# Optimization experiments

Hardware: AMD Instinct MI355X
Metric: run time of the kernel (lower is better)

The kernel has to match this reference:

```python
import jax, jax.numpy as jnp
import numpy as np
from jax import lax

C = 512
BN_EPS = 1e-5
GLN_EPS = 1e-8


def setup_inputs() -> dict:
    key = jax.random.key(0)
    ks = jax.random.split(key, 10)
    B, T = 16, 4000
    x = jax.random.normal(ks[0], (B, C, T), dtype=jnp.float32)
    # BatchNorm1d params (eval mode: affine + running stats)
    bn_gamma = jax.random.normal(ks[1], (C,), dtype=jnp.float32) * 0.1 + 1.0
    bn_beta = jax.random.normal(ks[2], (C,), dtype=jnp.float32) * 0.1
    bn_mean = jax.random.normal(ks[3], (C,), dtype=jnp.float32) * 0.1
    bn_var = jax.random.uniform(ks[4], (C,), dtype=jnp.float32) + 0.5
    # depthwise Conv1d(512,512,3,groups=512,bias=False): kernel [O=C, I=1, K=3]
    dw_w = jax.random.normal(ks[5], (C, 1, 3), dtype=jnp.float32) * (1.0 / np.sqrt(3.0))
    # PReLU default: single shared parameter init 0.25
    prelu_a = jnp.full((1,), 0.25, dtype=jnp.float32)
    # GlobalLayerNorm(512) affine params
    gln_gamma = jnp.ones((C,), dtype=jnp.float32)
    gln_beta = jnp.zeros((C,), dtype=jnp.float32)
    # pointwise Conv1d(512,512,1,bias=False): weight [O, I]
    pw_w = jax.random.normal(ks[6], (C, C), dtype=jnp.float32) * (1.0 / np.sqrt(C))
    return {"x": x, "bn_gamma": bn_gamma, "bn_beta": bn_beta, "bn_mean": bn_mean,
            "bn_var": bn_var, "dw_w": dw_w, "prelu_a": prelu_a,
            "gln_gamma": gln_gamma, "gln_beta": gln_beta, "pw_w": pw_w}


def reference(x, bn_gamma, bn_beta, bn_mean, bn_var, dw_w, prelu_a,
              gln_gamma, gln_beta, pw_w):
    # ReLU
    h = jax.nn.relu(x)
    # BatchNorm1d (eval mode, running stats), per-channel affine over [B,C,T]
    scale = (bn_gamma * lax.rsqrt(bn_var + BN_EPS))[None, :, None]
    h = h * scale + (bn_beta - bn_mean * bn_gamma * lax.rsqrt(bn_var + BN_EPS))[None, :, None]
    # depthwise conv1d, kernel 3, pad 1, groups=C
    h = lax.conv_general_dilated(h, dw_w, window_strides=(1,), padding=((1, 1),),
                                 feature_group_count=C,
                                 dimension_numbers=("NCH", "OIH", "NCH"))
    # PReLU (single shared slope)
    h = jnp.where(h >= 0, h, prelu_a[0] * h)
    # GlobalLayerNorm: normalize over (C, T) per sample, per-channel affine
    mean = jnp.mean(h, axis=(1, 2), keepdims=True)
    var = jnp.mean(jnp.square(h - mean), axis=(1, 2), keepdims=True)
    h = gln_gamma[None, :, None] * (h - mean) * lax.rsqrt(var + GLN_EPS) + gln_beta[None, :, None]
    # pointwise 1x1 conv == channel GEMM
    h = jnp.einsum("oc,bct->bot", pw_w, h)
    # residual
    return h + x
```

## Files before the change

kernel.cpp:

```cpp
#include <hip/hip_runtime.h>
#include <stdint.h>

#define B_ 16
#define C_ 512
#define T_ 4000
#define TPAD 4096

typedef float f32x4 __attribute__((ext_vector_type(4)));
typedef __bf16 bf16x8 __attribute__((ext_vector_type(8)));

__device__ inline unsigned short f2b(float f) {
  uint32_t u = __builtin_bit_cast(uint32_t, f);
  u = (u + 0x7fffu + ((u >> 16) & 1u)) >> 16;
  return (unsigned short)u;
}
__device__ inline float b2f(unsigned short h) {
  uint32_t u = ((uint32_t)h) << 16;
  return __builtin_bit_cast(float, u);
}
__device__ inline void gl_lds16(const void* g, void* s) {
  __builtin_amdgcn_global_load_lds(
      (const __attribute__((address_space(1))) uint32_t*)g,
      (__attribute__((address_space(3))) uint32_t*)s, 16, 0, 0);
}


__global__ void k_init(float* wsf) {
  int i = threadIdx.x;
  if (i < 32) wsf[i] = 0.f;
}

__global__ __launch_bounds__(64) void k_prepw(const float* __restrict__ pw,
                                              const float* __restrict__ gamma,
                                              const float* __restrict__ beta,
                                              unsigned short* __restrict__ Wp,
                                              float* __restrict__ wsf) {
  int o = blockIdx.x, l = threadIdx.x;
  float a1 = 0.f, a2 = 0.f;
  for (int j = 0; j < 8; ++j) {
    int c = j * 64 + l;
    float wv = pw[o * 512 + c];
    unsigned short wb = f2b(wv * gamma[c]);
    Wp[o * 512 + c] = wb;
    a1 += b2f(wb);
    a2 += wv * beta[c];
  }
  for (int s = 32; s > 0; s >>= 1) { a1 += __shfl_down(a1, s); a2 += __shfl_down(a2, s); }
  if (l == 0) { wsf[64 + o] = a1; wsf[576 + o] = a2; }
}

__global__ __launch_bounds__(512) void k_front(const float* __restrict__ x,
    const float* __restrict__ bng, const float* __restrict__ bnb,
    const float* __restrict__ bnm, const float* __restrict__ bnv,
    const float* __restrict__ dw, const float* __restrict__ pa,
    unsigned short* __restrict__ hT, float* __restrict__ wsf) {
  __shared__ unsigned short hs[256 * 128] __attribute__((aligned(16)));
  __shared__ float psc[128], pbi[128], pq0[128], pq1[128], pq2[128];
  __shared__ float partial[16];
  int tid = threadIdx.x;
  int l = tid & 63, w = tid >> 6;
  int tb = blockIdx.x;
  int cb = blockIdx.y;
  int b  = blockIdx.z;
  int t0 = tb * 256;
  if (tid < 128) {
    int c = cb * 128 + tid;
    float sc = bng[c] * rsqrtf(bnv[c] + 1e-5f);
    psc[tid] = sc;
    pbi[tid] = bnb[c] - bnm[c] * sc;
    pq0[tid] = dw[3 * c];
    pq1[tid] = dw[3 * c + 1];
    pq2[tid] = dw[3 * c + 2];
  }
  float alpha = pa[0];
  __syncthreads();

  int t = t0 + 4 * l;
  bool full = (t + 3 < T_);
  bool has_l = (t0 > 0);
  bool has_r = (t0 + 256 < T_);
  float sum = 0.f, sq = 0.f;
  int cs_x = (l & 7) << 3;

#pragma unroll 2
  for (int i = 0; i < 16; ++i) {
    int cl = w * 16 + i;
    const float* xr = x + ((size_t)b * C_ + cb * 128 + cl) * T_;
    float sc = psc[cl], bi = pbi[cl];
    float w0 = pq0[cl], w1 = pq1[cl], w2 = pq2[cl];
    f32x4 u;
    if (full) {
      const f32x4 v = *(const f32x4*)(xr + t);
      u.x = fmaxf(v.x, 0.f) * sc + bi;
      u.y = fmaxf(v.y, 0.f) * sc + bi;
      u.z = fmaxf(v.z, 0.f) * sc + bi;
      u.w = fmaxf(v.w, 0.f) * sc + bi;
    } else {
      u = (f32x4){0.f, 0.f, 0.f, 0.f};
    }
    float el = has_l ? (fmaxf(xr[t0 - 1], 0.f) * sc + bi) : 0.f;
    float er = has_r ? (fmaxf(xr[t0 + 256], 0.f) * sc + bi) : 0.f;
    float up = __shfl_up(u.w, 1);   if (l == 0)  up = el;
    float un = __shfl_down(u.x, 1); if (l == 63) un = er;
    float h[4];
    h[0] = w0 * up  + w1 * u.x + w2 * u.y;
    h[1] = w0 * u.x + w1 * u.y + w2 * u.z;
    h[2] = w0 * u.y + w1 * u.z + w2 * u.w;
    h[3] = w0 * u.z + w1 * u.w + w2 * un;
    int cs = cl ^ cs_x;
#pragma unroll
    for (int j = 0; j < 4; ++j) {
      float p = h[j] >= 0.f ? h[j] : alpha * h[j];
      if (!full) p = 0.f;
      sum += p; sq += p * p;
      hs[(4 * l + j) * 128 + cs] = f2b(p);
    }
  }

  for (int s = 32; s > 0; s >>= 1) { sum += __shfl_down(sum, s); sq += __shfl_down(sq, s); }
  if (l == 0) { partial[w] = sum; partial[8 + w] = sq; }
  __syncthreads();
  if (tid == 0) {
    float a = 0.f, c2 = 0.f;
    for (int k = 0; k < 8; ++k) { a += partial[k]; c2 += partial[8 + k]; }
    atomicAdd(&wsf[b], a);
    atomicAdd(&wsf[16 + b], c2);
  }

  unsigned short* dstb = hT + ((size_t)b * TPAD + t0) * 512 + cb * 128;
#pragma unroll
  for (int p = 0; p < 8; ++p) {
    int idx = p * 512 + tid;
    int tl = idx >> 4, g = idx & 15;
    int gs = g ^ ((tl >> 2) & 7);
    uint4 val = *(const uint4*)(hs + tl * 128 + gs * 8);
    *(uint4*)(dstb + (size_t)tl * 512 + g * 8) = val;
  }
}

__global__ void k_finalize(float* wsf) {
  int b = threadIdx.x;
  if (b < 16) {
    float n = (float)C_ * (float)T_;
    float mean = wsf[b] / n;
    float var = wsf[16 + b] / n - mean * mean;
    wsf[32 + b] = mean;
    wsf[48 + b] = rsqrtf(fmaxf(var, 0.f) + 1e-8f);
  }
}

__global__ __launch_bounds__(512, 2) void k_gemm(const unsigned short* __restrict__ Wp,
    const unsigned short* __restrict__ hT, const float* __restrict__ x,
    const float* __restrict__ wsf, float* __restrict__ out) {
  __shared__ unsigned short As0[8192], As1[8192], Bs0[8192], Bs1[8192];
  int tid = threadIdx.x;
  int l = tid & 63, w = tid >> 6;
  int nb = blockIdx.x, mb = blockIdx.y, b = blockIdx.z;
  int wm = w >> 2, wn = w & 3;
  const unsigned short* hTb = hT + (size_t)b * TPAD * 512;

  int aoff[2], boff[2], ldso[2];
#pragma unroll
  for (int r = 0; r < 2; ++r) {
    int i = r * 512 + tid;
    int row = i >> 2, s = i & 3;
    int ksl = (s ^ ((row >> 1) & 3)) << 3;
    aoff[r] = (mb * 256 + row) * 512 + ksl;
    boff[r] = (nb * 256 + row) * 512 + ksl;
    ldso[r] = i * 8;
  }

  int aro[8], bro[4];
#pragma unroll
  for (int fm = 0; fm < 8; ++fm) {
    int row = wm * 128 + fm * 16 + (l & 15);
    int slot = (l >> 4) ^ ((row >> 1) & 3);
    aro[fm] = row * 32 + slot * 8;
  }
#pragma unroll
  for (int fn = 0; fn < 4; ++fn) {
    int row = wn * 64 + fn * 16 + (l & 15);
    int slot = (l >> 4) ^ ((row >> 1) & 3);
    bro[fn] = row * 32 + slot * 8;
  }

  const unsigned short *cA = As0, *cB = Bs0;
  unsigned short *nA = As1, *nB = Bs1;

#pragma unroll
  for (int r = 0; r < 2; ++r) {
    gl_lds16(Wp + aoff[r], As0 + ldso[r]);
    gl_lds16(hTb + boff[r], Bs0 + ldso[r]);
  }
  __syncthreads();

  f32x4 acc[8][4] = {};
#pragma unroll 1
  for (int kt = 0; kt < 16; ++kt) {
    if (kt < 15) {
      int kofs = (kt + 1) * 32;
#pragma unroll
      for (int r = 0; r < 2; ++r) {
        gl_lds16(Wp + aoff[r] + kofs, nA + ldso[r]);
        gl_lds16(hTb + boff[r] + kofs, nB + ldso[r]);
      }
    }
    bf16x8 af[8], bfv[4];
#pragma unroll
    for (int fm = 0; fm < 8; ++fm) af[fm] = *(const bf16x8*)(cA + aro[fm]);
#pragma unroll
    for (int fn = 0; fn < 4; ++fn) bfv[fn] = *(const bf16x8*)(cB + bro[fn]);
    __builtin_amdgcn_s_setprio(1);
#pragma unroll
    for (int fm = 0; fm < 8; ++fm)
#pragma unroll
      for (int fn = 0; fn < 4; ++fn)
        acc[fm][fn] = __builtin_amdgcn_mfma_f32_16x16x32_bf16(af[fm], bfv[fn], acc[fm][fn], 0, 0, 0);
    __builtin_amdgcn_s_setprio(0);
    __syncthreads();
    const unsigned short* t1 = cA; cA = nA; nA = (unsigned short*)t1;
    const unsigned short* t2 = cB; cB = nB; nB = (unsigned short*)t2;
  }

  float mean = wsf[32 + b], rstd = wsf[48 + b];
  float mr = mean * rstd;
#pragma unroll
  for (int fm = 0; fm < 8; ++fm) {
    int o0 = mb * 256 + wm * 128 + fm * 16 + ((l >> 4) << 2);
    float bias[4];
#pragma unroll
    for (int j = 0; j < 4; ++j) {
      int o = o0 + j;
      bias[j] = wsf[576 + o] - mr * wsf[64 + o];
    }
#pragma unroll
    for (int fn = 0; fn < 4; ++fn) {
      int t = nb * 256 + wn * 64 + fn * 16 + (l & 15);
      if (t < T_) {
#pragma unroll
        for (int j = 0; j < 4; ++j) {
          int o = o0 + j;
          size_t idx = ((size_t)b * C_ + o) * T_ + t;
          out[idx] = rstd * acc[fm][fn][j] + bias[j] + x[idx];
        }
      }
    }
  }
}

extern "C" void kernel_launch(void* const* d_in, const int* in_sizes, int n_in,
                              void* d_out, int out_size, void* d_ws, size_t ws_size,
                              hipStream_t stream) {
  const float* x   = (const float*)d_in[0];
  const float* bng = (const float*)d_in[1];
  const float* bnb = (const float*)d_in[2];
  const float* bnm = (const float*)d_in[3];
  const float* bnv = (const float*)d_in[4];
  const float* dw  = (const float*)d_in[5];
  const float* pa  = (const float*)d_in[6];
  const float* gg  = (const float*)d_in[7];
  const float* gb  = (const float*)d_in[8];
  const float* pw  = (const float*)d_in[9];
  float* out = (float*)d_out;
  float* wsf = (float*)d_ws;
  unsigned short* Wp = (unsigned short*)((char*)d_ws + 8192);
  unsigned short* hT = (unsigned short*)((char*)d_ws + (1 << 20));

  k_init<<<dim3(1), dim3(64), 0, stream>>>(wsf);
  k_prepw<<<dim3(512), dim3(64), 0, stream>>>(pw, gg, gb, Wp, wsf);
  k_front<<<dim3(16, 4, 16), dim3(512), 0, stream>>>(x, bng, bnb, bnm, bnv, dw, pa, hT, wsf);
  k_finalize<<<dim3(1), dim3(64), 0, stream>>>(wsf);
  k_gemm<<<dim3(16, 2, 16), dim3(512), 0, stream>>>(Wp, hT, x, wsf, out);
}
```

Measured before the change: 153.9 us.

## Prefetch two K-tiles ahead with explicit vmcnt waits in GEMM loop

Restructures the GEMM main loop so two global-to-LDS tiles are in flight. Each iteration waits only on the older loads (vmcnt(4)), reads fragments into registers, then issues the next prefetch into the buffer just consumed. This replaces the full __syncthreads, which drained all memory ops, and aims to hide global load latency behind the MFMA work. The cost is two raw barriers per iteration and reliance on hand-counted waitcnt values, which would break if the number of loads per tile changed.

```diff
diff --git a/kernel.cpp b/kernel.cpp
--- a/kernel.cpp
+++ b/kernel.cpp
@@ -184,42 +184,52 @@
     bro[fn] = row * 32 + slot * 8;
   }
 
-  const unsigned short *cA = As0, *cB = Bs0;
-  unsigned short *nA = As1, *nB = Bs1;
-
 #pragma unroll
   for (int r = 0; r < 2; ++r) {
     gl_lds16(Wp + aoff[r], As0 + ldso[r]);
     gl_lds16(hTb + boff[r], Bs0 + ldso[r]);
   }
-  __syncthreads();
+#pragma unroll
+  for (int r = 0; r < 2; ++r) {
+    gl_lds16(Wp + aoff[r] + 32, As1 + ldso[r]);
+    gl_lds16(hTb + boff[r] + 32, Bs1 + ldso[r]);
+  }
+
+  unsigned short *cA = As0, *cB = Bs0;
+  unsigned short *oA = As1, *oB = Bs1;
 
   f32x4 acc[8][4] = {};
 #pragma unroll 1
   for (int kt = 0; kt < 16; ++kt) {
-    if (kt < 15) {
-      int kofs = (kt + 1) * 32;
+    if (kt == 15) asm volatile("s_waitcnt vmcnt(0)" ::: "memory");
+    else          asm volatile("s_waitcnt vmcnt(4)" ::: "memory");
+    __builtin_amdgcn_s_barrier();
+    __builtin_amdgcn_sched_barrier(0);
+    bf16x8 af[8], bv[4];
+#pragma unroll
+    for (int fm = 0; fm < 8; ++fm) af[fm] = *(const bf16x8*)(cA + aro[fm]);
+#pragma unroll
+    for (int fn = 0; fn < 4; ++fn) bv[fn] = *(const bf16x8*)(cB + bro[fn]);
+    asm volatile("s_waitcnt lgkmcnt(0)" ::: "memory");
+    __builtin_amdgcn_s_barrier();
+    __builtin_amdgcn_sched_barrier(0);
+    if (kt < 14) {
+      int kofs = (kt + 2) * 32;
 #pragma unroll
       for (int r = 0; r < 2; ++r) {
-        gl_lds16(Wp + aoff[r] + kofs, nA + ldso[r]);
-        gl_lds16(hTb + boff[r] + kofs, nB + ldso[r]);
+        gl_lds16(Wp + aoff[r] + kofs, cA + ldso[r]);
+        gl_lds16(hTb + boff[r] + kofs, cB + ldso[r]);
       }
     }
-    bf16x8 af[8], bfv[4];
-#pragma unroll
-    for (int fm = 0; fm < 8; ++fm) af[fm] = *(const bf16x8*)(cA + aro[fm]);
-#pragma unroll
-    for (int fn = 0; fn < 4; ++fn) bfv[fn] = *(const bf16x8*)(cB + bro[fn]);
     __builtin_amdgcn_s_setprio(1);
 #pragma unroll
     for (int fm = 0; fm < 8; ++fm)
 #pragma unroll
       for (int fn = 0; fn < 4; ++fn)
-        acc[fm][fn] = __builtin_amdgcn_mfma_f32_16x16x32_bf16(af[fm], bfv[fn], acc[fm][fn], 0, 0, 0);
+        acc[fm][fn] = __builtin_amdgcn_mfma_f32_16x16x32_bf16(af[fm], bv[fn], acc[fm][fn], 0, 0, 0);
     __builtin_amdgcn_s_setprio(0);
-    __syncthreads();
-    const unsigned short* t1 = cA; cA = nA; nA = (unsigned short*)t1;
-    const unsigned short* t2 = cB; cB = nB; nB = (unsigned short*)t2;
+    unsigned short* t1 = cA; cA = oA; oA = t1;
+    unsigned short* t2 = cB; cB = oB; oB = t2;
   }
 
   float mean = wsf[32 + b], rstd = wsf[48 + b];
```

Measured after the change: 159.8 us. 3.8% more time.
